# Performance work log

Measured on AMD Instinct MI355X. Metric: run time of the kernel, lower is better.

## Reference

```python
import jax, jax.numpy as jnp
import numpy as np

HIDDEN = 64

def gcn_conv(x, W, b, src, dst, num_nodes):
    # GCNConv: out = D^{-1/2} (A + I) D^{-1/2} (x @ W) + b
    h = x @ W                                            # [N, F_out]
    ones = jnp.ones(src.shape[0], dtype=x.dtype)
    deg = jax.ops.segment_sum(ones, dst, num_segments=num_nodes) + 1.0  # +1 for self-loop
    dinv = jax.lax.rsqrt(deg)                             # deg^{-1/2}, deg >= 1 so safe
    norm = dinv[src] * dinv[dst]                          # [E]
    msgs = h[src] * norm[:, None]                         # [E, F_out]
    agg = jax.ops.segment_sum(msgs, dst, num_segments=num_nodes)
    # self-loop contribution: norm for (i,i) edge = dinv[i]^2
    out = agg + h * (dinv * dinv)[:, None] + b
    return out


def setup_inputs() -> dict:
    key = jax.random.key(0)
    k1, k2, k3, k4, k5 = jax.random.split(key, 5)
    N, F_in, F_out, E = 50000, 256, 128, 1600000
    x = jax.random.normal(k1, (N, F_in), dtype=jnp.float32)
    edge_index = jax.random.randint(k2, (2, E), 0, N, dtype=jnp.int64)
    W1 = jax.random.normal(k3, (F_in, HIDDEN), dtype=jnp.float32) * (1.0 / np.sqrt(F_in))
    b1 = jnp.zeros((HIDDEN,), dtype=jnp.float32)
    W2 = jax.random.normal(k4, (HIDDEN, F_out), dtype=jnp.float32) * (1.0 / np.sqrt(HIDDEN))
    b2 = jnp.zeros((F_out,), dtype=jnp.float32)
    return {"x": x, "edge_index": edge_index, "W1": W1, "b1": b1, "W2": W2, "b2": b2}


def reference(x, edge_index, W1, b1, W2, b2):
    num_nodes = x.shape[0]
    src, dst = edge_index[0], edge_index[1]
    h = gcn_conv(x, W1, b1, src, dst, num_nodes)
    h = jax.nn.relu(h)
    # dropout is identity in eval mode (training=False)
    out = gcn_conv(h, W2, b2, src, dst, num_nodes)
    return out
```

## Files before the change

kernel.cpp:

```cpp
#include <hip/hip_runtime.h>

#define FI 256
#define FH 64
#define FO 128
#define ASORT_CHUNK 2048

typedef __attribute__((ext_vector_type(8))) short bf16x8;
typedef __attribute__((ext_vector_type(4))) float f32x4;

__device__ __forceinline__ ushort f2bf(float x) {
    unsigned b = __float_as_uint(x);
    b += 0x7fffu + ((b >> 16) & 1u);
    return (ushort)(b >> 16);
}
__device__ __forceinline__ float bf2f(ushort u) {
    return __uint_as_float(((unsigned)u) << 16);
}


__global__ void zero_i32(int* __restrict__ p, int n) {
    int i = blockIdx.x * 256 + threadIdx.x;
    if (i < n) p[i] = 0;
}

__global__ void deg_cnt_kernel(const int* __restrict__ dst, int* __restrict__ cnt, int E) {
    int base = blockIdx.x * 1024 + threadIdx.x;
    #pragma unroll
    for (int q = 0; q < 4; ++q) {
        int e = base + q * 256;
        if (e < E) atomicAdd(&cnt[dst[e]], 1);
    }
}

__global__ void dinv_kernel(const int* __restrict__ cnt, float* __restrict__ dinv, int N) {
    int i = blockIdx.x * 256 + threadIdx.x;
    if (i < N) dinv[i] = rsqrtf((float)cnt[i] + 1.0f);
}


__global__ __launch_bounds__(256) void hist_part_kernel(const int* __restrict__ dst,
                                                        int* __restrict__ bucket_cnt, int E) {
    __shared__ int lcnt[256];
    int t = threadIdx.x;
    int base = blockIdx.x * ASORT_CHUNK;
    lcnt[t] = 0;
    __syncthreads();
    #pragma unroll
    for (int j = 0; j < 8; ++j) {
        int e = base + j * 256 + t;
        if (e < E) atomicAdd(&lcnt[((unsigned)dst[e]) >> 8], 1);
    }
    __syncthreads();
    int v = lcnt[t];
    if (v > 0) atomicAdd(&bucket_cnt[t], v);
}

__global__ __launch_bounds__(256) void bucket_scan_kernel(const int* __restrict__ bucket_cnt,
                                                          int* __restrict__ bucket_base,
                                                          int* __restrict__ bucket_pos, int E) {
    __shared__ int sc[256];
    int t = threadIdx.x;
    int sum = bucket_cnt[t];
    sc[t] = sum;
    __syncthreads();
    for (int off = 1; off < 256; off <<= 1) {
        int u = (t >= off) ? sc[t - off] : 0;
        __syncthreads();
        sc[t] += u;
        __syncthreads();
    }
    int excl = sc[t] - sum;
    bucket_base[t] = excl;
    bucket_pos[t]  = excl;
    if (t == 255) bucket_base[256] = sc[255];
}

__global__ __launch_bounds__(256) void binA_kernel(const int* __restrict__ src,
                                                   const int* __restrict__ dst,
                                                   int* __restrict__ bucket_pos,
                                                   unsigned* __restrict__ binned, int E) {
    __shared__ int lcnt[256];
    __shared__ int lbase[256];
    __shared__ int gbase[256];
    __shared__ int sc[256];
    __shared__ unsigned sorted[ASORT_CHUNK];
    int t = threadIdx.x;
    int base = blockIdx.x * ASORT_CHUNK;
    lcnt[t] = 0;
    __syncthreads();
    unsigned pk[8];
    short bb[8];
    short mi[8];
    #pragma unroll
    for (int j = 0; j < 8; ++j) {
        int e = base + j * 256 + t;
        if (e < E) {
            unsigned s = (unsigned)src[e];
            unsigned d = (unsigned)dst[e];
            pk[j] = s | (d << 16);
            int b = (int)(d >> 8);
            bb[j] = (short)b;
            mi[j] = (short)atomicAdd(&lcnt[b], 1);
        } else {
            bb[j] = -1;
        }
    }
    __syncthreads();
    int v = lcnt[t];
    sc[t] = v;
    __syncthreads();
    #pragma unroll
    for (int off = 1; off < 256; off <<= 1) {
        int u = (t >= off) ? sc[t - off] : 0;
        __syncthreads();
        sc[t] += u;
        __syncthreads();
    }
    lbase[t] = sc[t] - v;
    if (v > 0) gbase[t] = atomicAdd(&bucket_pos[t], v);
    __syncthreads();
    #pragma unroll
    for (int j = 0; j < 8; ++j)
        if (bb[j] >= 0) sorted[lbase[(int)bb[j]] + (int)mi[j]] = pk[j];
    int tot = sc[255];
    __syncthreads();
    for (int i = t; i < tot; i += 256) {
        unsigned vv = sorted[i];
        int b = (int)(vv >> 24);
        binned[gbase[b] + (i - lbase[b])] = vv;
    }
}

__global__ __launch_bounds__(256) void binB_kernel(const int* __restrict__ bucket_base,
                                                   const unsigned* __restrict__ binned,
                                                   int* __restrict__ rec4,
                                                   int* __restrict__ row_start,
                                                   int* __restrict__ cnt,
                                                   float* __restrict__ dinv, int N) {
    __shared__ int lcnt[256];
    __shared__ int sc[256];
    __shared__ int lstart[256];
    __shared__ int loff[256];
    int t = threadIdx.x;
    int d0 = blockIdx.x << 8;
    int start = bucket_base[blockIdx.x];
    int end   = bucket_base[blockIdx.x + 1];
    lcnt[t] = 0;
    __syncthreads();
    for (int i = start + t; i < end; i += 256)
        atomicAdd(&lcnt[(binned[i] >> 16) & 0xffu], 1);
    __syncthreads();
    int v = lcnt[t];
    sc[t] = v;
    __syncthreads();
    for (int off = 1; off < 256; off <<= 1) {
        int u = (t >= off) ? sc[t - off] : 0;
        __syncthreads();
        sc[t] += u;
        __syncthreads();
    }
    int st = start + sc[t] - v;
    lstart[t] = st;
    loff[t] = 0;
    if (d0 + t < N) {
        row_start[d0 + t] = st;
        cnt[d0 + t] = v;
        dinv[d0 + t] = rsqrtf((float)v + 1.0f);
    }
    __syncthreads();
    int i = start + t;
    for (; i + 768 < end; i += 1024) {
        unsigned v0 = binned[i];
        unsigned v1 = binned[i + 256];
        unsigned v2 = binned[i + 512];
        unsigned v3 = binned[i + 768];
        int dA = (int)((v0 >> 16) & 0xffu); int kA = atomicAdd(&loff[dA], 1);
        rec4[lstart[dA] + kA] = (int)(v0 & 0xffffu);
        int dB = (int)((v1 >> 16) & 0xffu); int kB = atomicAdd(&loff[dB], 1);
        rec4[lstart[dB] + kB] = (int)(v1 & 0xffffu);
        int dC = (int)((v2 >> 16) & 0xffu); int kC = atomicAdd(&loff[dC], 1);
        rec4[lstart[dC] + kC] = (int)(v2 & 0xffffu);
        int dD = (int)((v3 >> 16) & 0xffu); int kD = atomicAdd(&loff[dD], 1);
        rec4[lstart[dD] + kD] = (int)(v3 & 0xffffu);
    }
    for (; i < end; i += 256) {
        unsigned v4 = binned[i];
        int d = (int)((v4 >> 16) & 0xffu);
        int k = atomicAdd(&loff[d], 1);
        rec4[lstart[d] + k] = (int)(v4 & 0xffffu);
    }
}


#define ACC8(hv, wt)                                                   \
    acc[0] = fmaf(__uint_as_float((hv).x << 16),         wt, acc[0]);  \
    acc[1] = fmaf(__uint_as_float((hv).x & 0xffff0000u), wt, acc[1]);  \
    acc[2] = fmaf(__uint_as_float((hv).y << 16),         wt, acc[2]);  \
    acc[3] = fmaf(__uint_as_float((hv).y & 0xffff0000u), wt, acc[3]);  \
    acc[4] = fmaf(__uint_as_float((hv).z << 16),         wt, acc[4]);  \
    acc[5] = fmaf(__uint_as_float((hv).z & 0xffff0000u), wt, acc[5]);  \
    acc[6] = fmaf(__uint_as_float((hv).w << 16),         wt, acc[6]);  \
    acc[7] = fmaf(__uint_as_float((hv).w & 0xffff0000u), wt, acc[7]);

#define GATHER_CHUNK(OFFS)                                                     \
    for (int c0 = 0; c0 < n; c0 += 64) {                                       \
        int idx_l = c0 + L;                                                    \
        int sreg = node;                                                       \
        float wreg = 0.f;                                                      \
        if (idx_l < n) {                                                       \
            sreg = rec4[beg + idx_l];                                          \
            wreg = dinv[sreg] * dvd;                                           \
        }                                                                      \
        int m = n - c0; if (m > 64) m = 64;                                    \
        int umax = (m + 7) >> 3;                                               \
        uint4 hv[8];                                                           \
        _Pragma("unroll")                                                      \
        for (int u = 0; u < 8; ++u) {                                          \
            if (u < umax) {                                                    \
                int sidx = __shfl(sreg, u * 8 + g, 64);                        \
                hv[u] = *(const uint4*)(hb + (size_t)sidx * 256 + (OFFS) + q * 8); \
            }                                                                  \
        }                                                                      \
        _Pragma("unroll")                                                      \
        for (int u = 0; u < 8; ++u) {                                          \
            if (u < umax) {                                                    \
                float wt = __shfl(wreg, u * 8 + g, 64);                        \
                ACC8(hv[u], wt)                                                \
            }                                                                  \
        }                                                                      \
    }

__global__ void gather_relu_kernel(const int* __restrict__ rec4, const int* __restrict__ row_start,
                                   const int* __restrict__ cnt, const float* __restrict__ dinv,
                                   const float* __restrict__ b1, float* __restrict__ out, int N) {
    int node = blockIdx.x * 4 + (threadIdx.x >> 6);
    if (node >= N) return;
    int L = threadIdx.x & 63;
    int g = L >> 3;
    int q = L & 7;
    const ushort* hb = (const ushort*)out;
    int beg = row_start[node];
    int n   = cnt[node];
    float dvd = dinv[node];
    float acc[8] = {0.f, 0.f, 0.f, 0.f, 0.f, 0.f, 0.f, 0.f};
    GATHER_CHUNK(128)
    #pragma unroll
    for (int off = 8; off < 64; off <<= 1)
        #pragma unroll
        for (int j = 0; j < 8; ++j)
            acc[j] += __shfl_xor(acc[j], off, 64);
    if (L < 8) {
        float dv2 = dvd * dvd;
        uint4 ho = *(const uint4*)(hb + (size_t)node * 256 + 128 + q * 8);
        float4 bl = *(const float4*)&b1[q * 8];
        float4 bh = *(const float4*)&b1[q * 8 + 4];
        float r0 = fmaxf(acc[0] + dv2 * __uint_as_float(ho.x << 16)         + bl.x, 0.f);
        float r1 = fmaxf(acc[1] + dv2 * __uint_as_float(ho.x & 0xffff0000u) + bl.y, 0.f);
        float r2 = fmaxf(acc[2] + dv2 * __uint_as_float(ho.y << 16)         + bl.z, 0.f);
        float r3 = fmaxf(acc[3] + dv2 * __uint_as_float(ho.y & 0xffff0000u) + bl.w, 0.f);
        float r4 = fmaxf(acc[4] + dv2 * __uint_as_float(ho.z << 16)         + bh.x, 0.f);
        float r5 = fmaxf(acc[5] + dv2 * __uint_as_float(ho.z & 0xffff0000u) + bh.y, 0.f);
        float r6 = fmaxf(acc[6] + dv2 * __uint_as_float(ho.w << 16)         + bh.z, 0.f);
        float r7 = fmaxf(acc[7] + dv2 * __uint_as_float(ho.w & 0xffff0000u) + bh.w, 0.f);
        uint4 st;
        st.x = (unsigned)f2bf(r0) | ((unsigned)f2bf(r1) << 16);
        st.y = (unsigned)f2bf(r2) | ((unsigned)f2bf(r3) << 16);
        st.z = (unsigned)f2bf(r4) | ((unsigned)f2bf(r5) << 16);
        st.w = (unsigned)f2bf(r6) | ((unsigned)f2bf(r7) << 16);
        *(uint4*)((ushort*)out + (size_t)node * 256 + 192 + q * 8) = st;
    }
}

__global__ void gather_comb_kernel(const int* __restrict__ rec4, const int* __restrict__ row_start,
                                   const int* __restrict__ cnt, const float* __restrict__ dinv,
                                   float* __restrict__ out, int N) {
    int node = blockIdx.x * 4 + (threadIdx.x >> 6);
    if (node >= N) return;
    int L = threadIdx.x & 63;
    int g = L >> 3;
    int q = L & 7;
    const ushort* hb = (const ushort*)out;
    int beg = row_start[node];
    int n   = cnt[node];
    float dvd = dinv[node];
    float acc[8] = {0.f, 0.f, 0.f, 0.f, 0.f, 0.f, 0.f, 0.f};
    GATHER_CHUNK(192)
    #pragma unroll
    for (int off = 8; off < 64; off <<= 1)
        #pragma unroll
        for (int j = 0; j < 8; ++j)
            acc[j] += __shfl_xor(acc[j], off, 64);
    if (L < 8) {
        float dv2 = dvd * dvd;
        uint4 ho = *(const uint4*)(hb + (size_t)node * 256 + 192 + q * 8);
        float4 o0, o1;
        o0.x = acc[0] + dv2 * __uint_as_float(ho.x << 16);
        o0.y = acc[1] + dv2 * __uint_as_float(ho.x & 0xffff0000u);
        o0.z = acc[2] + dv2 * __uint_as_float(ho.y << 16);
        o0.w = acc[3] + dv2 * __uint_as_float(ho.y & 0xffff0000u);
        o1.x = acc[4] + dv2 * __uint_as_float(ho.z << 16);
        o1.y = acc[5] + dv2 * __uint_as_float(ho.z & 0xffff0000u);
        o1.z = acc[6] + dv2 * __uint_as_float(ho.w << 16);
        o1.w = acc[7] + dv2 * __uint_as_float(ho.w & 0xffff0000u);
        *(float4*)&out[(size_t)node * FO + q * 8]     = o0;
        *(float4*)&out[(size_t)node * FO + q * 8 + 4] = o1;
    }
}


__global__ __launch_bounds__(256) void mm1_mfma(const float* __restrict__ x,
                                                const float* __restrict__ W1,
                                                float* __restrict__ out, int N) {
    __shared__ short bfH[2048 * 8];
    __shared__ short bfL[2048 * 8];
    int tid = threadIdx.x;

    for (int e = tid; e < 2048; e += 256) {
        int l  = e & 63;
        int ct = e >> 6;
        int c  = ct >> 3, t = ct & 7;
        int col = c * 16 + (l & 15);
        int kb  = t * 32 + (l >> 4) * 8;
        #pragma unroll
        for (int j = 0; j < 8; ++j) {
            float wv = W1[(size_t)(kb + j) * 64 + col];
            ushort h = f2bf(wv);
            bfH[e * 8 + j] = (short)h;
            bfL[e * 8 + j] = (short)f2bf(wv - bf2f(h));
        }
    }
    __syncthreads();

    int wid = tid >> 6;
    int l   = tid & 63;
    int R0  = blockIdx.x * 128;
    int rowA = R0 + wid * 32 + (l & 15);
    int rowB = rowA + 16;
    int kg   = l >> 4;
    const float* xrA = x + (size_t)rowA * FI;
    const float* xrB = x + (size_t)rowB * FI;
    bool okA = rowA < N, okB = rowB < N;
    const float4 z4 = make_float4(0.f, 0.f, 0.f, 0.f);

    f32x4 acc[2][4];
    #pragma unroll
    for (int i = 0; i < 2; ++i)
        #pragma unroll
        for (int c = 0; c < 4; ++c) acc[i][c] = (f32x4){0.f, 0.f, 0.f, 0.f};

    for (int t = 0; t < 8; ++t) {
        int kb = t * 32 + kg * 8;
        float4 a0 = okA ? *(const float4*)&xrA[kb]     : z4;
        float4 a1 = okA ? *(const float4*)&xrA[kb + 4] : z4;
        float4 b0 = okB ? *(const float4*)&xrB[kb]     : z4;
        float4 b1 = okB ? *(const float4*)&xrB[kb + 4] : z4;
        bf16x8 ahA, alA, ahB, alB;
        {
            float va[8] = {a0.x, a0.y, a0.z, a0.w, a1.x, a1.y, a1.z, a1.w};
            float vb[8] = {b0.x, b0.y, b0.z, b0.w, b1.x, b1.y, b1.z, b1.w};
            #pragma unroll
            for (int j = 0; j < 8; ++j) {
                ushort h1v = f2bf(va[j]);
                ahA[j] = (short)h1v;
                alA[j] = (short)f2bf(va[j] - bf2f(h1v));
                ushort h2v = f2bf(vb[j]);
                ahB[j] = (short)h2v;
                alB[j] = (short)f2bf(vb[j] - bf2f(h2v));
            }
        }
        #pragma unroll
        for (int c = 0; c < 4; ++c) {
            int e = (c * 8 + t) * 64 + l;
            bf16x8 bh = *(const bf16x8*)&bfH[e * 8];
            bf16x8 bl = *(const bf16x8*)&bfL[e * 8];
            acc[0][c] = __builtin_amdgcn_mfma_f32_16x16x32_bf16(ahA, bh, acc[0][c], 0, 0, 0);
            acc[0][c] = __builtin_amdgcn_mfma_f32_16x16x32_bf16(ahA, bl, acc[0][c], 0, 0, 0);
            acc[0][c] = __builtin_amdgcn_mfma_f32_16x16x32_bf16(alA, bh, acc[0][c], 0, 0, 0);
            acc[1][c] = __builtin_amdgcn_mfma_f32_16x16x32_bf16(ahB, bh, acc[1][c], 0, 0, 0);
            acc[1][c] = __builtin_amdgcn_mfma_f32_16x16x32_bf16(ahB, bl, acc[1][c], 0, 0, 0);
            acc[1][c] = __builtin_amdgcn_mfma_f32_16x16x32_bf16(alB, bh, acc[1][c], 0, 0, 0);
        }
    }
    #pragma unroll
    for (int i = 0; i < 2; ++i) {
        int rbase = R0 + wid * 32 + i * 16 + (l >> 4) * 4;
        #pragma unroll
        for (int r = 0; r < 4; ++r) {
            int row = rbase + r;
            if (row < N) {
                ushort* ob = (ushort*)out + (size_t)row * 256 + 128;
                #pragma unroll
                for (int c = 0; c < 4; ++c)
                    ob[c * 16 + (l & 15)] = f2bf(acc[i][c][r]);
            }
        }
    }
}

__global__ __launch_bounds__(256) void mm2_tiled(const float* __restrict__ W2,
                                                 const float* __restrict__ b2,
                                                 float* __restrict__ out, int N) {
    __shared__ float xs[64][68];
    __shared__ float ws[64][128];
    int tid = threadIdx.x;
    int R0  = blockIdx.x * 64;
    int ty  = tid >> 4;
    int tx  = tid & 15;

    {
        int sr = tid >> 2;
        int l4 = tid & 3;
        int grow = R0 + sr;
        bool ok = grow < N;
        const float* orow = out + (size_t)grow * FO;
        #pragma unroll
        for (int q = 0; q < 4; ++q) {
            int j0 = (l4 + 4 * q) * 4;
            float4 a = ok ? *(const float4*)&orow[j0] : make_float4(0.f, 0.f, 0.f, 0.f);
            xs[j0 + 0][sr] = a.x;
            xs[j0 + 1][sr] = a.y;
            xs[j0 + 2][sr] = a.z;
            xs[j0 + 3][sr] = a.w;
        }
    }
    #pragma unroll
    for (int q = 0; q < 8; ++q) {
        int f = tid + q * 256;
        *(float4*)&ws[f >> 5][(f & 31) * 4] = *(const float4*)&W2[(size_t)f * 4];
    }
    __syncthreads();

    float acc[4][8];
    #pragma unroll
    for (int i = 0; i < 4; ++i)
        #pragma unroll
        for (int j = 0; j < 8; ++j) acc[i][j] = 0.f;

    #pragma unroll 4
    for (int k = 0; k < FH; ++k) {
        float4 a  = *(const float4*)&xs[k][ty * 4];
        float4 bl = *(const float4*)&ws[k][tx * 4];
        float4 bh = *(const float4*)&ws[k][64 + tx * 4];
        float av[4] = {a.x, a.y, a.z, a.w};
        float bv[8] = {bl.x, bl.y, bl.z, bl.w, bh.x, bh.y, bh.z, bh.w};
        #pragma unroll
        for (int i = 0; i < 4; ++i)
            #pragma unroll
            for (int j = 0; j < 8; ++j)
                acc[i][j] = fmaf(av[i], bv[j], acc[i][j]);
    }

    float4 b2l = *(const float4*)&b2[tx * 4];
    float4 b2h = *(const float4*)&b2[64 + tx * 4];
    #pragma unroll
    for (int i = 0; i < 4; ++i) {
        int row = R0 + ty * 4 + i;
        if (row < N) {
            float* o = out + (size_t)row * FO;
            *(float4*)&o[tx * 4] = make_float4(acc[i][0] + b2l.x, acc[i][1] + b2l.y,
                                               acc[i][2] + b2l.z, acc[i][3] + b2l.w);
            *(float4*)&o[64 + tx * 4] = make_float4(acc[i][4] + b2h.x, acc[i][5] + b2h.y,
                                                    acc[i][6] + b2h.z, acc[i][7] + b2h.w);
        }
    }
}


__global__ void expand_hs1_kernel(float* __restrict__ out, int N) {
    int row = blockIdx.x * 4 + (threadIdx.x >> 6);
    if (row >= N) return;
    int lane = threadIdx.x & 63;
    float v = bf2f(((const ushort*)out)[(size_t)row * 256 + 128 + lane]);
    out[(size_t)row * FO + FH + lane] = v;
}

__global__ void zero_half_kernel(float* __restrict__ out, int half, int N) {
    int i = blockIdx.x * 256 + threadIdx.x;
    if (i >= N * FH) return;
    out[(size_t)(i >> 6) * FO + half + (i & 63)] = 0.f;
}

__global__ void scatter_half_kernel(const int* __restrict__ src, const int* __restrict__ dst,
                                    const float* __restrict__ dinv, float* __restrict__ out,
                                    int rh, int wh, int E) {
    int e = blockIdx.x * 4 + (threadIdx.x >> 6);
    if (e >= E) return;
    int lane = threadIdx.x & 63;
    int s = src[e];
    int d = dst[e];
    float w = dinv[s] * dinv[d];
    atomicAdd(&out[(size_t)d * FO + wh + lane], out[(size_t)s * FO + rh + lane] * w);
}

__global__ void finish1_kernel(float* __restrict__ out, const float* __restrict__ dinv,
                               const float* __restrict__ b1, int N) {
    int i = blockIdx.x * 256 + threadIdx.x;
    if (i >= N * FH) return;
    int row = i >> 6;
    int c   = i & 63;
    size_t base = (size_t)row * FO;
    float dv = dinv[row];
    out[base + c] = fmaxf(out[base + c] + dv * dv * out[base + FH + c] + b1[c], 0.f);
}

__global__ void finish2_kernel(float* __restrict__ out, const float* __restrict__ dinv, int N) {
    int i = blockIdx.x * 256 + threadIdx.x;
    if (i >= N * FH) return;
    int row = i >> 6;
    int c   = i & 63;
    size_t base = (size_t)row * FO;
    float dv = dinv[row];
    out[base + c] = out[base + FH + c] + dv * dv * out[base + c];
}

extern "C" void kernel_launch(void* const* d_in, const int* in_sizes, int n_in,
                              void* d_out, int out_size, void* d_ws, size_t ws_size,
                              hipStream_t stream) {
    const float* x  = (const float*)d_in[0];
    const int*   ei = (const int*)d_in[1];
    const float* W1 = (const float*)d_in[2];
    const float* b1 = (const float*)d_in[3];
    const float* W2 = (const float*)d_in[4];
    const float* b2 = (const float*)d_in[5];
    float* out = (float*)d_out;

    int N = in_sizes[0] / FI;
    int E = in_sizes[1] / 2;
    const int* src = ei;
    const int* dst = ei + E;

    char* w = (char*)d_ws;
    float* dinv        = (float*)w;      w += (size_t)N * 4;
    int*   cnt         = (int*)w;        w += (size_t)N * 4;
    int*   row_start   = (int*)w;        w += (size_t)N * 4;
    int*   bucket_cnt  = (int*)w;        w += 256 * 4;
    int*   bucket_pos  = (int*)w;        w += 256 * 4;
    int*   bucket_base = (int*)w;        w += 260 * 4;
    unsigned* binned   = (unsigned*)w;   w += (size_t)E * 4;
    int*   rec4        = (int*)w;        w += (size_t)E * 4;
    size_t need = (size_t)(w - (char*)d_ws);

    int nblkA = (E + ASORT_CHUNK - 1) / ASORT_CHUNK;
    int nbk   = (N + 255) >> 8;

    if (ws_size >= need && N <= 65536) {
        zero_i32<<<1, 256, 0, stream>>>(bucket_cnt, 256);
        hist_part_kernel<<<nblkA, 256, 0, stream>>>(dst, bucket_cnt, E);
        bucket_scan_kernel<<<1, 256, 0, stream>>>(bucket_cnt, bucket_base, bucket_pos, E);
        binA_kernel<<<nblkA, 256, 0, stream>>>(src, dst, bucket_pos, binned, E);
        binB_kernel<<<nbk, 256, 0, stream>>>(bucket_base, binned, rec4, row_start, cnt, dinv, N);

        mm1_mfma<<<(N + 127) / 128, 256, 0, stream>>>(x, W1, out, N);
        gather_relu_kernel<<<(N + 3) / 4, 256, 0, stream>>>(rec4, row_start, cnt, dinv, b1, out, N);
        gather_comb_kernel<<<(N + 3) / 4, 256, 0, stream>>>(rec4, row_start, cnt, dinv, out, N);
        mm2_tiled<<<(N + 63) / 64, 256, 0, stream>>>(W2, b2, out, N);
    } else {
        zero_i32<<<(N + 255) / 256, 256, 0, stream>>>(cnt, N);
        deg_cnt_kernel<<<(E + 1023) / 1024, 256, 0, stream>>>(dst, cnt, E);
        dinv_kernel<<<(N + 255) / 256, 256, 0, stream>>>(cnt, dinv, N);
        mm1_mfma<<<(N + 127) / 128, 256, 0, stream>>>(x, W1, out, N);
        expand_hs1_kernel<<<(N + 3) / 4, 256, 0, stream>>>(out, N);
        zero_half_kernel<<<((N * FH) + 255) / 256, 256, 0, stream>>>(out, 0, N);
        scatter_half_kernel<<<(E + 3) / 4, 256, 0, stream>>>(src, dst, dinv, out, FH, 0, E);
        finish1_kernel<<<((N * FH) + 255) / 256, 256, 0, stream>>>(out, dinv, b1, N);
        zero_half_kernel<<<((N * FH) + 255) / 256, 256, 0, stream>>>(out, FH, N);
        scatter_half_kernel<<<(E + 3) / 4, 256, 0, stream>>>(src, dst, dinv, out, 0, FH, E);
        finish2_kernel<<<((N * FH) + 255) / 256, 256, 0, stream>>>(out, dinv, N);
        mm2_tiled<<<(N + 63) / 64, 256, 0, stream>>>(W2, b2, out, N);
    }
}
```

Measured before the change: 277.5 us.

## Use 512-thread blocks in mm1 with one row tile per wave and prefetch

```diff
diff --git a/kernel.cpp b/kernel.cpp
--- a/kernel.cpp
+++ b/kernel.cpp
@@ -308,25 +308,27 @@
 }
 
 
-__global__ __launch_bounds__(256) void mm1_mfma(const float* __restrict__ x,
+__global__ __launch_bounds__(512) void mm1_mfma(const float* __restrict__ x,
                                                 const float* __restrict__ W1,
                                                 float* __restrict__ out, int N) {
     __shared__ short bfH[2048 * 8];
     __shared__ short bfL[2048 * 8];
     int tid = threadIdx.x;
 
-    for (int e = tid; e < 2048; e += 256) {
-        int l  = e & 63;
-        int ct = e >> 6;
-        int c  = ct >> 3, t = ct & 7;
-        int col = c * 16 + (l & 15);
-        int kb  = t * 32 + (l >> 4) * 8;
-        #pragma unroll
-        for (int j = 0; j < 8; ++j) {
-            float wv = W1[(size_t)(kb + j) * 64 + col];
-            ushort h = f2bf(wv);
-            bfH[e * 8 + j] = (short)h;
-            bfL[e * 8 + j] = (short)f2bf(wv - bf2f(h));
+    #pragma unroll
+    for (int i = 0; i < 8; ++i) {
+        int f = i * 512 + tid;
+        float4 wv = *(const float4*)&W1[(size_t)f * 4];
+        int k  = f >> 4;
+        int c4 = f & 15;
+        int j  = k & 7;
+        int e0 = ((c4 >> 2) * 8 + (k >> 5)) * 64 + ((k >> 3) & 3) * 16 + (c4 & 3) * 4;
+        float vv[4] = {wv.x, wv.y, wv.z, wv.w};
+        #pragma unroll
+        for (int cc = 0; cc < 4; ++cc) {
+            ushort h = f2bf(vv[cc]);
+            bfH[(e0 + cc) * 8 + j] = (short)h;
+            bfL[(e0 + cc) * 8 + j] = (short)f2bf(vv[cc] - bf2f(h));
         }
     }
     __syncthreads();
@@ -334,56 +336,48 @@
     int wid = tid >> 6;
     int l   = tid & 63;
     int R0  = blockIdx.x * 128;
-    int rowA = R0 + wid * 32 + (l & 15);
-    int rowB = rowA + 16;
+    int rowA = R0 + wid * 16 + (l & 15);
     int kg   = l >> 4;
-    const float* xrA = x + (size_t)rowA * FI;
-    const float* xrB = x + (size_t)rowB * FI;
-    bool okA = rowA < N, okB = rowB < N;
+    const float* xr = x + (size_t)rowA * FI;
+    bool ok = rowA < N;
     const float4 z4 = make_float4(0.f, 0.f, 0.f, 0.f);
 
-    f32x4 acc[2][4];
-    #pragma unroll
-    for (int i = 0; i < 2; ++i)
-        #pragma unroll
-        for (int c = 0; c < 4; ++c) acc[i][c] = (f32x4){0.f, 0.f, 0.f, 0.f};
-
+    f32x4 acc[4];
+    #pragma unroll
+    for (int c = 0; c < 4; ++c) acc[c] = (f32x4){0.f, 0.f, 0.f, 0.f};
+
+    float4 xa = ok ? *(const float4*)&xr[kg * 8]     : z4;
+    float4 xb = ok ? *(const float4*)&xr[kg * 8 + 4] : z4;
+
+    #pragma unroll
     for (int t = 0; t < 8; ++t) {
-        int kb = t * 32 + kg * 8;
-        float4 a0 = okA ? *(const float4*)&xrA[kb]     : z4;
-        float4 a1 = okA ? *(const float4*)&xrA[kb + 4] : z4;
-        float4 b0 = okB ? *(const float4*)&xrB[kb]     : z4;
-        float4 b1 = okB ? *(const float4*)&xrB[kb + 4] : z4;
-        bf16x8 ahA, alA, ahB, alB;
+        bf16x8 ah, al;
         {
-            float va[8] = {a0.x, a0.y, a0.z, a0.w, a1.x, a1.y, a1.z, a1.w};
-            float vb[8] = {b0.x, b0.y, b0.z, b0.w, b1.x, b1.y, b1.z, b1.w};
+            float va[8] = {xa.x, xa.y, xa.z, xa.w, xb.x, xb.y, xb.z, xb.w};
             #pragma unroll
             for (int j = 0; j < 8; ++j) {
-                ushort h1v = f2bf(va[j]);
-                ahA[j] = (short)h1v;
-                alA[j] = (short)f2bf(va[j] - bf2f(h1v));
-                ushort h2v = f2bf(vb[j]);
-                ahB[j] = (short)h2v;
-                alB[j] = (short)f2bf(vb[j] - bf2f(h2v));
+                ushort h = f2bf(va[j]);
+                ah[j] = (short)h;
+                al[j] = (short)f2bf(va[j] - bf2f(h));
             }
+        }
+        if (t < 7) {
+            int kb = (t + 1) * 32 + kg * 8;
+            xa = ok ? *(const float4*)&xr[kb]     : z4;
+            xb = ok ? *(const float4*)&xr[kb + 4] : z4;
         }
         #pragma unroll
         for (int c = 0; c < 4; ++c) {
             int e = (c * 8 + t) * 64 + l;
             bf16x8 bh = *(const bf16x8*)&bfH[e * 8];
             bf16x8 bl = *(const bf16x8*)&bfL[e * 8];
-            acc[0][c] = __builtin_amdgcn_mfma_f32_16x16x32_bf16(ahA, bh, acc[0][c], 0, 0, 0);
-            acc[0][c] = __builtin_amdgcn_mfma_f32_16x16x32_bf16(ahA, bl, acc[0][c], 0, 0, 0);
-            acc[0][c] = __builtin_amdgcn_mfma_f32_16x16x32_bf16(alA, bh, acc[0][c], 0, 0, 0);
-            acc[1][c] = __builtin_amdgcn_mfma_f32_16x16x32_bf16(ahB, bh, acc[1][c], 0, 0, 0);
-            acc[1][c] = __builtin_amdgcn_mfma_f32_16x16x32_bf16(ahB, bl, acc[1][c], 0, 0, 0);
-            acc[1][c] = __builtin_amdgcn_mfma_f32_16x16x32_bf16(alB, bh, acc[1][c], 0, 0, 0);
-        }
-    }
-    #pragma unroll
-    for (int i = 0; i < 2; ++i) {
-        int rbase = R0 + wid * 32 + i * 16 + (l >> 4) * 4;
+            acc[c] = __builtin_amdgcn_mfma_f32_16x16x32_bf16(ah, bh, acc[c], 0, 0, 0);
+            acc[c] = __builtin_amdgcn_mfma_f32_16x16x32_bf16(ah, bl, acc[c], 0, 0, 0);
+            acc[c] = __builtin_amdgcn_mfma_f32_16x16x32_bf16(al, bh, acc[c], 0, 0, 0);
+        }
+    }
+    {
+        int rbase = R0 + wid * 16 + (l >> 4) * 4;
         #pragma unroll
         for (int r = 0; r < 4; ++r) {
             int row = rbase + r;
@@ -391,7 +385,7 @@
                 ushort* ob = (ushort*)out + (size_t)row * 256 + 128;
                 #pragma unroll
                 for (int c = 0; c < 4; ++c)
-                    ob[c * 16 + (l & 15)] = f2bf(acc[i][c][r]);
+                    ob[c * 16 + (l & 15)] = f2bf(acc[c][r]);
             }
         }
     }
@@ -550,7 +544,7 @@
         binA_kernel<<<nblkA, 256, 0, stream>>>(src, dst, bucket_pos, binned, E);
         binB_kernel<<<nbk, 256, 0, stream>>>(bucket_base, binned, rec4, row_start, cnt, dinv, N);
 
-        mm1_mfma<<<(N + 127) / 128, 256, 0, stream>>>(x, W1, out, N);
+        mm1_mfma<<<(N + 127) / 128, 512, 0, stream>>>(x, W1, out, N);
         gather_relu_kernel<<<(N + 3) / 4, 256, 0, stream>>>(rec4, row_start, cnt, dinv, b1, out, N);
         gather_comb_kernel<<<(N + 3) / 4, 256, 0, stream>>>(rec4, row_start, cnt, dinv, out, N);
         mm2_tiled<<<(N + 63) / 64, 256, 0, stream>>>(W2, b2, out, N);
@@ -558,7 +552,7 @@
         zero_i32<<<(N + 255) / 256, 256, 0, stream>>>(cnt, N);
         deg_cnt_kernel<<<(E + 1023) / 1024, 256, 0, stream>>>(dst, cnt, E);
         dinv_kernel<<<(N + 255) / 256, 256, 0, stream>>>(cnt, dinv, N);
-        mm1_mfma<<<(N + 127) / 128, 256, 0, stream>>>(x, W1, out, N);
+        mm1_mfma<<<(N + 127) / 128, 512, 0, stream>>>(x, W1, out, N);
         expand_hs1_kernel<<<(N + 3) / 4, 256, 0, stream>>>(out, N);
         zero_half_kernel<<<((N * FH) + 255) / 256, 256, 0, stream>>>(out, 0, N);
         scatter_half_kernel<<<(E + 3) / 4, 256, 0, stream>>>(src, dst, dinv, out, FH, 0, E);
```

After: 277.2 us. About the same (-0.1%).
